# Kernel tuning notes

Measured on AMD Instinct MI355X. Metric: run time of the kernel, lower is better.

The kernel has to match this reference:

```python
import jax, jax.numpy as jnp
import numpy as np

B, S, H, NH = 4, 2048, 1024, 16
HD = H // NH

def setup_inputs() -> dict:
    key = jax.random.key(0)
    ks = jax.random.split(key, 9)
    s = 1.0 / np.sqrt(H)
    return {
        "x": jax.random.normal(ks[0], (B, S, H), dtype=jnp.float32),
        "Wq": jax.random.uniform(ks[1], (H, H), jnp.float32, -s, s),
        "bq": jax.random.uniform(ks[2], (H,), jnp.float32, -s, s),
        "Wk": jax.random.uniform(ks[3], (H, H), jnp.float32, -s, s),
        "bk": jax.random.uniform(ks[4], (H,), jnp.float32, -s, s),
        "Wv": jax.random.uniform(ks[5], (H, H), jnp.float32, -s, s),
        "bv": jax.random.uniform(ks[6], (H,), jnp.float32, -s, s),
        "Wo": jax.random.uniform(ks[7], (H, H), jnp.float32, -s, s),
        "bo": jax.random.uniform(ks[8], (H,), jnp.float32, -s, s),
    }

def reference(x, Wq, bq, Wk, bk, Wv, bv, Wo, bo):
    b, s, h = x.shape
    scale = np.sqrt(HD).astype(np.float32)
    def split_heads(t):  # [b,s,h] -> [b,nh,s,hd]
        return t.reshape(b, s, NH, HD).transpose(0, 2, 1, 3)
    Q = split_heads(x @ Wq.T + bq)
    K = split_heads(x @ Wk.T + bk)
    V = split_heads(x @ Wv.T + bv)
    scores = jnp.einsum('bnqd,bnkd->bnqk', Q, K) / scale
    weights = jax.nn.softmax(scores, axis=-1)
    attn = jnp.einsum('bnqk,bnkd->bnqd', weights, V)
    attn = attn.transpose(0, 2, 1, 3).reshape(b, s, h)
    return attn @ Wo.T + bo
```

## Files before the change

### kernel.cpp

```cpp
#include <hip/hip_runtime.h>
#include <cstdint>

#define BB 4
#define SS 2048
#define HH 1024
#define NHH 16
#define HDD 64

typedef __bf16 bf16x8 __attribute__((ext_vector_type(8)));
typedef float f32x4 __attribute__((ext_vector_type(4)));
typedef unsigned short u16x8 __attribute__((ext_vector_type(8)));

__device__ __forceinline__ unsigned short f2b(float f) {
    unsigned int u = __float_as_uint(f);
    u += 0x7fffu + ((u >> 16) & 1u);
    return (unsigned short)(u >> 16);
}

__device__ __forceinline__ void gload_lds16(const void* g, void* l) {
    __builtin_amdgcn_global_load_lds(
        (const __attribute__((address_space(1))) void*)g,
        (__attribute__((address_space(3))) void*)l, 16, 0, 0);
}

__global__ void cvt_bf16(const float* __restrict__ in,
                         unsigned short* __restrict__ out, long n) {
    long i = ((long)blockIdx.x * blockDim.x + threadIdx.x) * 4;
    long stride = (long)gridDim.x * blockDim.x * 4;
    for (; i < n; i += stride) {
        float4 v = *reinterpret_cast<const float4*>(in + i);
        ushort4 o;
        o.x = f2b(v.x); o.y = f2b(v.y); o.z = f2b(v.z); o.w = f2b(v.w);
        *reinterpret_cast<ushort4*>(out + i) = o;
    }
}

__global__ void cvt_w4(const float* __restrict__ w0, const float* __restrict__ w1,
                       const float* __restrict__ w2, const float* __restrict__ w3,
                       unsigned short* __restrict__ out) {
    const float* s = blockIdx.y == 0 ? w0 : blockIdx.y == 1 ? w1 : blockIdx.y == 2 ? w2 : w3;
    unsigned short* o = out + (size_t)blockIdx.y * ((size_t)HH * HH);
    long n = (long)HH * HH;
    long stride = (long)gridDim.x * blockDim.x * 4;
    for (long i = ((long)blockIdx.x * blockDim.x + threadIdx.x) * 4; i < n; i += stride) {
        float4 v = *reinterpret_cast<const float4*>(s + i);
        ushort4 w;
        w.x = f2b(v.x); w.y = f2b(v.y); w.z = f2b(v.z); w.w = f2b(v.w);
        *reinterpret_cast<ushort4*>(o + i) = w;
    }
}

template<int MODE>
__global__ __launch_bounds__(256) void gemm_bt(
    const unsigned short* __restrict__ A,
    const unsigned short* __restrict__ Bm,
    const float* __restrict__ bias,
    void* __restrict__ Cout,
    int M, int N, int K)
{
    __shared__ alignas(16) unsigned short Al[128][32];
    __shared__ alignas(16) unsigned short Bl[128][32];

    const int tid = threadIdx.x;
    const int lane = tid & 63;
    const int wid  = tid >> 6;
    const int wm = wid >> 1, wn = wid & 1;
    const int l15 = lane & 15, g = lane >> 4;
    const int row0 = blockIdx.y * 128, col0 = blockIdx.x * 128;

    f32x4 acc[4][4];
#pragma unroll
    for (int i = 0; i < 4; i++)
#pragma unroll
        for (int j = 0; j < 4; j++) acc[i][j] = (f32x4)0.0f;

    const int off0 = tid * 16;
    const int r0s = off0 >> 6, cb0 = off0 & 63;
    const int off1 = off0 + 4096;
    const int r1s = off1 >> 6, cb1 = off1 & 63;

    for (int k0 = 0; k0 < K; k0 += 32) {
        const char* gA = (const char*)(A + (size_t)row0 * K + k0);
        const char* gB = (const char*)(Bm + (size_t)col0 * K + k0);
        char* lA = (char*)&Al[0][0] + wid * 1024;
        char* lB = (char*)&Bl[0][0] + wid * 1024;
        gload_lds16(gA + (size_t)r0s * (K * 2) + cb0, lA);
        gload_lds16(gA + (size_t)r1s * (K * 2) + cb1, lA + 4096);
        gload_lds16(gB + (size_t)r0s * (K * 2) + cb0, lB);
        gload_lds16(gB + (size_t)r1s * (K * 2) + cb1, lB + 4096);
        __syncthreads();

        bf16x8 af[4], bf[4];
#pragma unroll
        for (int i = 0; i < 4; i++)
            af[i] = *reinterpret_cast<const bf16x8*>(&Al[wm * 64 + i * 16 + l15][g * 8]);
#pragma unroll
        for (int j = 0; j < 4; j++)
            bf[j] = *reinterpret_cast<const bf16x8*>(&Bl[wn * 64 + j * 16 + l15][g * 8]);
        __builtin_amdgcn_s_setprio(1);
#pragma unroll
        for (int i = 0; i < 4; i++)
#pragma unroll
            for (int j = 0; j < 4; j++)
                acc[i][j] = __builtin_amdgcn_mfma_f32_16x16x32_bf16(af[i], bf[j], acc[i][j], 0, 0, 0);
        __builtin_amdgcn_s_setprio(0);
        __syncthreads();
    }

#pragma unroll
    for (int i = 0; i < 4; i++) {
#pragma unroll
        for (int j = 0; j < 4; j++) {
#pragma unroll
            for (int r = 0; r < 4; r++) {
                int row = row0 + wm * 64 + i * 16 + g * 4 + r;
                int col = col0 + wn * 64 + j * 16 + l15;
                float v = acc[i][j][r] + bias[col];
                if (MODE == 0) {
                    reinterpret_cast<unsigned short*>(Cout)[(size_t)row * N + col] = f2b(v);
                } else if (MODE == 1) {
                    int b = row >> 11;
                    int s = row & (SS - 1);
                    int s6 = s & 63;
                    int sp6 = (s6 & 0x23) | ((s6 & 0x0C) << 1) | ((s6 & 0x10) >> 2);
                    int head = col >> 6;
                    int d = col & (HDD - 1);
                    size_t idx = (((size_t)b * NHH + head) * HDD + d) * SS + (s & ~63) + sp6;
                    reinterpret_cast<unsigned short*>(Cout)[idx] = f2b(v);
                } else {
                    reinterpret_cast<float*>(Cout)[(size_t)row * N + col] = v;
                }
            }
        }
    }
}

__global__ __launch_bounds__(256, 4) void attn_kernel(
    const unsigned short* __restrict__ Q,
    const unsigned short* __restrict__ K,
    const unsigned short* __restrict__ Vt,
    unsigned short* __restrict__ Oa)
{
    __shared__ alignas(16) unsigned short Kl[2][64][72];
    __shared__ alignas(16) unsigned short Vl[2][64][72];

    const int tid = threadIdx.x;
    const int lane = tid & 63;
    const int wid  = tid >> 6;
    const int l15 = lane & 15, g = lane >> 4;

    const int b  = blockIdx.z;
    const int h  = blockIdx.y;
    const int q0 = blockIdx.x * 128;
    const int qA = q0 + wid * 32;

    const float qs = 0.125f * 1.44269504088896f;
    const unsigned short* qpA = Q + (size_t)(b * SS + qA + l15) * HH + h * HDD + g * 8;
    const unsigned short* qpB = qpA + (size_t)16 * HH;
    u16x8 ra0 = *reinterpret_cast<const u16x8*>(qpA);
    u16x8 ra1 = *reinterpret_cast<const u16x8*>(qpA + 32);
    u16x8 rb0 = *reinterpret_cast<const u16x8*>(qpB);
    u16x8 rb1 = *reinterpret_cast<const u16x8*>(qpB + 32);
#pragma unroll
    for (int j = 0; j < 8; j++) {
        ra0[j] = f2b(__uint_as_float((unsigned)ra0[j] << 16) * qs);
        ra1[j] = f2b(__uint_as_float((unsigned)ra1[j] << 16) * qs);
        rb0[j] = f2b(__uint_as_float((unsigned)rb0[j] << 16) * qs);
        rb1[j] = f2b(__uint_as_float((unsigned)rb1[j] << 16) * qs);
    }
    const bf16x8 qa0 = __builtin_bit_cast(bf16x8, ra0);
    const bf16x8 qa1 = __builtin_bit_cast(bf16x8, ra1);
    const bf16x8 qb0 = __builtin_bit_cast(bf16x8, rb0);
    const bf16x8 qb1 = __builtin_bit_cast(bf16x8, rb1);

    u16x8 ou;
#pragma unroll
    for (int j = 0; j < 8; j++) ou[j] = 0x3F80;
    const bf16x8 ones8 = __builtin_bit_cast(bf16x8, ou);
    const f32x4 zero4 = (f32x4)0.0f;

    f32x4 acc_a[4], acc_b[4];
#pragma unroll
    for (int dn = 0; dn < 4; dn++) { acc_a[dn] = zero4; acc_b[dn] = zero4; }
    float m_a = -INFINITY, m_b = -INFINITY, l_a = 0.f, l_b = 0.f;

    const int sr = tid >> 2;
    const int sc = (tid & 3) * 16;

    const unsigned short* gK = K  + (size_t)(b * SS + sr) * HH + h * HDD + sc;
    const unsigned short* gV = Vt + (((size_t)b * NHH + h) * HDD + sr) * SS + sc;

    int4 kr0, kr1, vr0, vr1;

    kr0 = *reinterpret_cast<const int4*>(gK);
    kr1 = *reinterpret_cast<const int4*>(gK + 8);
    vr0 = *reinterpret_cast<const int4*>(gV);
    vr1 = *reinterpret_cast<const int4*>(gV + 8);
    *reinterpret_cast<int4*>(&Kl[0][sr][sc])     = kr0;
    *reinterpret_cast<int4*>(&Kl[0][sr][sc + 8]) = kr1;
    *reinterpret_cast<int4*>(&Vl[0][sr][sc])     = vr0;
    *reinterpret_cast<int4*>(&Vl[0][sr][sc + 8]) = vr1;
    gK += (size_t)64 * HH;
    gV += 64;
    __syncthreads();

    const int NT = SS / 64;
    int cur = 0;

    for (int kt = 0; kt < NT; kt++) {
        if (kt + 1 < NT) {
            kr0 = *reinterpret_cast<const int4*>(gK);
            kr1 = *reinterpret_cast<const int4*>(gK + 8);
            vr0 = *reinterpret_cast<const int4*>(gV);
            vr1 = *reinterpret_cast<const int4*>(gV + 8);
            gK += (size_t)64 * HH;
            gV += 64;
        }

        f32x4 sa[4], sb[4];
        __builtin_amdgcn_s_setprio(1);
#pragma unroll
        for (int n = 0; n < 4; n++) {
            bf16x8 kf0 = *reinterpret_cast<const bf16x8*>(&Kl[cur][n * 16 + l15][g * 8]);
            bf16x8 kf1 = *reinterpret_cast<const bf16x8*>(&Kl[cur][n * 16 + l15][32 + g * 8]);
            sa[n] = __builtin_amdgcn_mfma_f32_16x16x32_bf16(kf0, qa0, zero4, 0, 0, 0);
            sa[n] = __builtin_amdgcn_mfma_f32_16x16x32_bf16(kf1, qa1, sa[n], 0, 0, 0);
            sb[n] = __builtin_amdgcn_mfma_f32_16x16x32_bf16(kf0, qb0, zero4, 0, 0, 0);
            sb[n] = __builtin_amdgcn_mfma_f32_16x16x32_bf16(kf1, qb1, sb[n], 0, 0, 0);
        }
        __builtin_amdgcn_s_setprio(0);

        bf16x8 pa0, pa1, pb0, pb1;
        {
            float u0 = fmaxf(fmaxf(sa[0][0], sa[0][1]), fmaxf(sa[0][2], sa[0][3]));
            float u1 = fmaxf(fmaxf(sa[1][0], sa[1][1]), fmaxf(sa[1][2], sa[1][3]));
            float u2 = fmaxf(fmaxf(sa[2][0], sa[2][1]), fmaxf(sa[2][2], sa[2][3]));
            float u3 = fmaxf(fmaxf(sa[3][0], sa[3][1]), fmaxf(sa[3][2], sa[3][3]));
            float mt = fmaxf(fmaxf(u0, u1), fmaxf(u2, u3));
            mt = fmaxf(mt, __shfl_xor(mt, 16));
            mt = fmaxf(mt, __shfl_xor(mt, 32));
            if (!__all(mt - m_a <= 8.0f)) {
                float mnew = fmaxf(m_a, mt);
                float scl = __builtin_amdgcn_exp2f(m_a - mnew);
                m_a = mnew; l_a *= scl;
#pragma unroll
                for (int dn = 0; dn < 4; dn++)
#pragma unroll
                    for (int r = 0; r < 4; r++) acc_a[dn][r] *= scl;
            }
            float p[4][4];
#pragma unroll
            for (int n = 0; n < 4; n++)
#pragma unroll
                for (int r = 0; r < 4; r++) p[n][r] = __builtin_amdgcn_exp2f(sa[n][r] - m_a);
#pragma unroll
            for (int j = 0; j < 8; j++) {
                pa0[j] = (__bf16)p[j >> 2][j & 3];
                pa1[j] = (__bf16)p[2 + (j >> 2)][j & 3];
            }
        }
        {
            float u0 = fmaxf(fmaxf(sb[0][0], sb[0][1]), fmaxf(sb[0][2], sb[0][3]));
            float u1 = fmaxf(fmaxf(sb[1][0], sb[1][1]), fmaxf(sb[1][2], sb[1][3]));
            float u2 = fmaxf(fmaxf(sb[2][0], sb[2][1]), fmaxf(sb[2][2], sb[2][3]));
            float u3 = fmaxf(fmaxf(sb[3][0], sb[3][1]), fmaxf(sb[3][2], sb[3][3]));
            float mt = fmaxf(fmaxf(u0, u1), fmaxf(u2, u3));
            mt = fmaxf(mt, __shfl_xor(mt, 16));
            mt = fmaxf(mt, __shfl_xor(mt, 32));
            if (!__all(mt - m_b <= 8.0f)) {
                float mnew = fmaxf(m_b, mt);
                float scl = __builtin_amdgcn_exp2f(m_b - mnew);
                m_b = mnew; l_b *= scl;
#pragma unroll
                for (int dn = 0; dn < 4; dn++)
#pragma unroll
                    for (int r = 0; r < 4; r++) acc_b[dn][r] *= scl;
            }
            float p[4][4];
#pragma unroll
            for (int n = 0; n < 4; n++)
#pragma unroll
                for (int r = 0; r < 4; r++) p[n][r] = __builtin_amdgcn_exp2f(sb[n][r] - m_b);
#pragma unroll
            for (int j = 0; j < 8; j++) {
                pb0[j] = (__bf16)p[j >> 2][j & 3];
                pb1[j] = (__bf16)p[2 + (j >> 2)][j & 3];
            }
        }

        f32x4 la = zero4, lb = zero4;
        __builtin_amdgcn_s_setprio(1);
#pragma unroll
        for (int ks = 0; ks < 2; ks++) {
            bf16x8 pA = ks ? pa1 : pa0;
            bf16x8 pB = ks ? pb1 : pb0;
#pragma unroll
            for (int dn = 0; dn < 4; dn++) {
                bf16x8 vf = *reinterpret_cast<const bf16x8*>(&Vl[cur][dn * 16 + l15][ks * 32 + g * 8]);
                acc_a[dn] = __builtin_amdgcn_mfma_f32_16x16x32_bf16(vf, pA, acc_a[dn], 0, 0, 0);
                acc_b[dn] = __builtin_amdgcn_mfma_f32_16x16x32_bf16(vf, pB, acc_b[dn], 0, 0, 0);
            }
        }
        la = __builtin_amdgcn_mfma_f32_16x16x32_bf16(ones8, pa0, la, 0, 0, 0);
        la = __builtin_amdgcn_mfma_f32_16x16x32_bf16(ones8, pa1, la, 0, 0, 0);
        lb = __builtin_amdgcn_mfma_f32_16x16x32_bf16(ones8, pb0, lb, 0, 0, 0);
        lb = __builtin_amdgcn_mfma_f32_16x16x32_bf16(ones8, pb1, lb, 0, 0, 0);
        __builtin_amdgcn_s_setprio(0);
        l_a += la[0];
        l_b += lb[0];

        if (kt + 1 < NT) {
            int nxt = cur ^ 1;
            *reinterpret_cast<int4*>(&Kl[nxt][sr][sc])     = kr0;
            *reinterpret_cast<int4*>(&Kl[nxt][sr][sc + 8]) = kr1;
            *reinterpret_cast<int4*>(&Vl[nxt][sr][sc])     = vr0;
            *reinterpret_cast<int4*>(&Vl[nxt][sr][sc + 8]) = vr1;
        }
        __syncthreads();
        cur ^= 1;
    }

    float inv_a = 1.0f / l_a;
    float inv_b = 1.0f / l_b;
    unsigned short* oA = Oa + (size_t)(b * SS + qA + l15) * HH + h * HDD;
    unsigned short* oB = oA + (size_t)16 * HH;
#pragma unroll
    for (int dn = 0; dn < 4; dn++) {
        ushort4 wa, wb;
        wa.x = f2b(acc_a[dn][0] * inv_a); wa.y = f2b(acc_a[dn][1] * inv_a);
        wa.z = f2b(acc_a[dn][2] * inv_a); wa.w = f2b(acc_a[dn][3] * inv_a);
        wb.x = f2b(acc_b[dn][0] * inv_b); wb.y = f2b(acc_b[dn][1] * inv_b);
        wb.z = f2b(acc_b[dn][2] * inv_b); wb.w = f2b(acc_b[dn][3] * inv_b);
        *reinterpret_cast<ushort4*>(oA + dn * 16 + g * 4) = wa;
        *reinterpret_cast<ushort4*>(oB + dn * 16 + g * 4) = wb;
    }
}

extern "C" void kernel_launch(void* const* d_in, const int* in_sizes, int n_in,
                              void* d_out, int out_size, void* d_ws, size_t ws_size,
                              hipStream_t stream) {
    const float* x  = (const float*)d_in[0];
    const float* Wq = (const float*)d_in[1];
    const float* bq = (const float*)d_in[2];
    const float* Wk = (const float*)d_in[3];
    const float* bk = (const float*)d_in[4];
    const float* Wv = (const float*)d_in[5];
    const float* bv = (const float*)d_in[6];
    const float* Wo = (const float*)d_in[7];
    const float* bo = (const float*)d_in[8];
    float* out = (float*)d_out;

    const int M = BB * SS;
    const long nx = (long)M * HH;

    unsigned char* ws = (unsigned char*)d_ws;
    unsigned short* xb  = (unsigned short*)(ws);
    unsigned short* Wqb = (unsigned short*)(ws + 16777216);
    unsigned short* Wkb = (unsigned short*)(ws + 16777216 + 2097152);
    unsigned short* Wvb = (unsigned short*)(ws + 16777216 + 2 * 2097152);
    unsigned short* Wob = (unsigned short*)(ws + 16777216 + 3 * 2097152);
    unsigned short* Qb  = (unsigned short*)(ws + 16777216 + 4 * 2097152);
    unsigned short* Kb  = (unsigned short*)(ws + 2 * 16777216 + 4 * 2097152);
    unsigned short* Vtb = (unsigned short*)(ws + 3 * 16777216 + 4 * 2097152);
    unsigned short* Ab  = (unsigned short*)(ws + 4 * 16777216 + 4 * 2097152);

    cvt_bf16<<<4096, 256, 0, stream>>>(x, xb, nx);
    cvt_w4<<<dim3(256, 4), 256, 0, stream>>>(Wq, Wk, Wv, Wo, Wqb);

    dim3 ggrid(HH / 128, M / 128);
    gemm_bt<0><<<ggrid, 256, 0, stream>>>(xb, Wqb, bq, Qb, M, HH, HH);
    gemm_bt<0><<<ggrid, 256, 0, stream>>>(xb, Wkb, bk, Kb, M, HH, HH);
    gemm_bt<1><<<ggrid, 256, 0, stream>>>(xb, Wvb, bv, Vtb, M, HH, HH);

    dim3 agrid(SS / 128, NHH, BB);
    attn_kernel<<<agrid, 256, 0, stream>>>(Qb, Kb, Vtb, Ab);

    gemm_bt<2><<<ggrid, 256, 0, stream>>>(Ab, Wob, bo, out, M, HH, HH);
}
```

Before: 222.7 us.

## Fuse QKV projections into one GEMM launch and fragment-order attention LDS tiles

The three separate Q/K/V projection GEMMs become a single launch over a 3x wider N dimension, relying on the contiguous bf16 Wq/Wk/Wv buffers and choosing bias and output layout per column block. This removes two kernel launches and the tail effects of three smaller grids. The attention kernel also stores K and V tiles in LDS in MFMA-fragment order, so each lane reads one contiguous 16-byte slot instead of doing padded row reads. The new LDS write pattern during staging could cause bank conflicts of its own.

```diff
diff --git a/kernel.cpp b/kernel.cpp
--- a/kernel.cpp
+++ b/kernel.cpp
@@ -50,12 +50,101 @@
     }
 }
 
-template<int MODE>
-__global__ __launch_bounds__(256) void gemm_bt(
+__global__ __launch_bounds__(256) void gemm_qkv(
+    const unsigned short* __restrict__ A,
+    const unsigned short* __restrict__ Bqkv,
+    const float* __restrict__ bq, const float* __restrict__ bk,
+    const float* __restrict__ bv,
+    unsigned short* __restrict__ Qo, unsigned short* __restrict__ Ko,
+    unsigned short* __restrict__ Vto)
+{
+    __shared__ alignas(16) unsigned short Al[128][32];
+    __shared__ alignas(16) unsigned short Bl[128][32];
+
+    const int tid = threadIdx.x;
+    const int lane = tid & 63;
+    const int wid  = tid >> 6;
+    const int wm = wid >> 1, wn = wid & 1;
+    const int l15 = lane & 15, g = lane >> 4;
+    const int row0 = blockIdx.y * 128;
+    const int col0 = blockIdx.x * 128;
+    const int nb = col0 >> 10;
+    const int cbase = col0 & 1023;
+    const float* bias = nb == 0 ? bq : nb == 1 ? bk : bv;
+    const int K = HH;
+
+    f32x4 acc[4][4];
+#pragma unroll
+    for (int i = 0; i < 4; i++)
+#pragma unroll
+        for (int j = 0; j < 4; j++) acc[i][j] = (f32x4)0.0f;
+
+    const int off0 = tid * 16;
+    const int r0s = off0 >> 6, cb0 = off0 & 63;
+    const int off1 = off0 + 4096;
+    const int r1s = off1 >> 6, cb1 = off1 & 63;
+
+    for (int k0 = 0; k0 < K; k0 += 32) {
+        const char* gA = (const char*)(A + (size_t)row0 * K + k0);
+        const char* gB = (const char*)(Bqkv + (size_t)col0 * K + k0);
+        char* lA = (char*)&Al[0][0] + wid * 1024;
+        char* lB = (char*)&Bl[0][0] + wid * 1024;
+        gload_lds16(gA + (size_t)r0s * (K * 2) + cb0, lA);
+        gload_lds16(gA + (size_t)r1s * (K * 2) + cb1, lA + 4096);
+        gload_lds16(gB + (size_t)r0s * (K * 2) + cb0, lB);
+        gload_lds16(gB + (size_t)r1s * (K * 2) + cb1, lB + 4096);
+        __syncthreads();
+
+        bf16x8 af[4], bf[4];
+#pragma unroll
+        for (int i = 0; i < 4; i++)
+            af[i] = *reinterpret_cast<const bf16x8*>(&Al[wm * 64 + i * 16 + l15][g * 8]);
+#pragma unroll
+        for (int j = 0; j < 4; j++)
+            bf[j] = *reinterpret_cast<const bf16x8*>(&Bl[wn * 64 + j * 16 + l15][g * 8]);
+        __builtin_amdgcn_s_setprio(1);
+#pragma unroll
+        for (int i = 0; i < 4; i++)
+#pragma unroll
+            for (int j = 0; j < 4; j++)
+                acc[i][j] = __builtin_amdgcn_mfma_f32_16x16x32_bf16(af[i], bf[j], acc[i][j], 0, 0, 0);
+        __builtin_amdgcn_s_setprio(0);
+        __syncthreads();
+    }
+
+#pragma unroll
+    for (int i = 0; i < 4; i++) {
+#pragma unroll
+        for (int j = 0; j < 4; j++) {
+#pragma unroll
+            for (int r = 0; r < 4; r++) {
+                int row = row0 + wm * 64 + i * 16 + g * 4 + r;
+                int col = cbase + wn * 64 + j * 16 + l15;
+                float v = acc[i][j][r] + bias[col];
+                if (nb == 0) {
+                    Qo[(size_t)row * HH + col] = f2b(v);
+                } else if (nb == 1) {
+                    Ko[(size_t)row * HH + col] = f2b(v);
+                } else {
+                    int b = row >> 11;
+                    int s = row & (SS - 1);
+                    int s6 = s & 63;
+                    int sp6 = (s6 & 0x23) | ((s6 & 0x0C) << 1) | ((s6 & 0x10) >> 2);
+                    int head = col >> 6;
+                    int d = col & (HDD - 1);
+                    size_t idx = (((size_t)b * NHH + head) * HDD + d) * SS + (s & ~63) + sp6;
+                    Vto[idx] = f2b(v);
+                }
+            }
+        }
+    }
+}
+
+__global__ __launch_bounds__(256) void gemm_out(
     const unsigned short* __restrict__ A,
     const unsigned short* __restrict__ Bm,
     const float* __restrict__ bias,
-    void* __restrict__ Cout,
+    float* __restrict__ Cout,
     int M, int N, int K)
 {
     __shared__ alignas(16) unsigned short Al[128][32];
@@ -115,21 +204,7 @@
             for (int r = 0; r < 4; r++) {
                 int row = row0 + wm * 64 + i * 16 + g * 4 + r;
                 int col = col0 + wn * 64 + j * 16 + l15;
-                float v = acc[i][j][r] + bias[col];
-                if (MODE == 0) {
-                    reinterpret_cast<unsigned short*>(Cout)[(size_t)row * N + col] = f2b(v);
-                } else if (MODE == 1) {
-                    int b = row >> 11;
-                    int s = row & (SS - 1);
-                    int s6 = s & 63;
-                    int sp6 = (s6 & 0x23) | ((s6 & 0x0C) << 1) | ((s6 & 0x10) >> 2);
-                    int head = col >> 6;
-                    int d = col & (HDD - 1);
-                    size_t idx = (((size_t)b * NHH + head) * HDD + d) * SS + (s & ~63) + sp6;
-                    reinterpret_cast<unsigned short*>(Cout)[idx] = f2b(v);
-                } else {
-                    reinterpret_cast<float*>(Cout)[(size_t)row * N + col] = v;
-                }
+                Cout[(size_t)row * N + col] = acc[i][j][r] + bias[col];
             }
         }
     }
@@ -141,8 +216,8 @@
     const unsigned short* __restrict__ Vt,
     unsigned short* __restrict__ Oa)
 {
-    __shared__ alignas(16) unsigned short Kl[2][64][72];
-    __shared__ alignas(16) unsigned short Vl[2][64][72];
+    __shared__ alignas(16) unsigned short Kf[2][8][64][8];
+    __shared__ alignas(16) unsigned short Vf[2][8][64][8];
 
     const int tid = threadIdx.x;
     const int lane = tid & 63;
@@ -184,22 +259,30 @@
     for (int dn = 0; dn < 4; dn++) { acc_a[dn] = zero4; acc_b[dn] = zero4; }
     float m_a = -INFINITY, m_b = -INFINITY, l_a = 0.f, l_b = 0.f;
 
-    const int sr = tid >> 2;
-    const int sc = (tid & 3) * 16;
-
-    const unsigned short* gK = K  + (size_t)(b * SS + sr) * HH + h * HDD + sc;
-    const unsigned short* gV = Vt + (((size_t)b * NHH + h) * HDD + sr) * SS + sc;
+    const int srow = tid >> 2;
+    const int d0a  = (tid & 3) * 2;
+    const int sfrag = ((srow >> 4) << 1) + (d0a >> 2);
+    const int sslot = (srow & 15) | ((d0a & 3) << 4);
+
+    const unsigned short* gK = K  + (size_t)(b * SS + srow) * HH + h * HDD + d0a * 8;
+    const unsigned short* gV = Vt + (((size_t)b * NHH + h) * HDD + srow) * SS + d0a * 8;
 
     int4 kr0, kr1, vr0, vr1;
+
+    auto stage_write = [&](int buf) {
+        unsigned short* pk = &Kf[buf][sfrag][0][0] + sslot * 8;
+        unsigned short* pv = &Vf[buf][sfrag][0][0] + sslot * 8;
+        *reinterpret_cast<int4*>(pk)       = kr0;
+        *reinterpret_cast<int4*>(pk + 128) = kr1;
+        *reinterpret_cast<int4*>(pv)       = vr0;
+        *reinterpret_cast<int4*>(pv + 128) = vr1;
+    };
 
     kr0 = *reinterpret_cast<const int4*>(gK);
     kr1 = *reinterpret_cast<const int4*>(gK + 8);
     vr0 = *reinterpret_cast<const int4*>(gV);
     vr1 = *reinterpret_cast<const int4*>(gV + 8);
-    *reinterpret_cast<int4*>(&Kl[0][sr][sc])     = kr0;
-    *reinterpret_cast<int4*>(&Kl[0][sr][sc + 8]) = kr1;
-    *reinterpret_cast<int4*>(&Vl[0][sr][sc])     = vr0;
-    *reinterpret_cast<int4*>(&Vl[0][sr][sc + 8]) = vr1;
+    stage_write(0);
     gK += (size_t)64 * HH;
     gV += 64;
     __syncthreads();
@@ -221,8 +304,8 @@
         __builtin_amdgcn_s_setprio(1);
 #pragma unroll
         for (int n = 0; n < 4; n++) {
-            bf16x8 kf0 = *reinterpret_cast<const bf16x8*>(&Kl[cur][n * 16 + l15][g * 8]);
-            bf16x8 kf1 = *reinterpret_cast<const bf16x8*>(&Kl[cur][n * 16 + l15][32 + g * 8]);
+            bf16x8 kf0 = *reinterpret_cast<const bf16x8*>(&Kf[cur][n * 2 + 0][lane][0]);
+            bf16x8 kf1 = *reinterpret_cast<const bf16x8*>(&Kf[cur][n * 2 + 1][lane][0]);
             sa[n] = __builtin_amdgcn_mfma_f32_16x16x32_bf16(kf0, qa0, zero4, 0, 0, 0);
             sa[n] = __builtin_amdgcn_mfma_f32_16x16x32_bf16(kf1, qa1, sa[n], 0, 0, 0);
             sb[n] = __builtin_amdgcn_mfma_f32_16x16x32_bf16(kf0, qb0, zero4, 0, 0, 0);
@@ -296,7 +379,7 @@
             bf16x8 pB = ks ? pb1 : pb0;
 #pragma unroll
             for (int dn = 0; dn < 4; dn++) {
-                bf16x8 vf = *reinterpret_cast<const bf16x8*>(&Vl[cur][dn * 16 + l15][ks * 32 + g * 8]);
+                bf16x8 vf = *reinterpret_cast<const bf16x8*>(&Vf[cur][dn * 2 + ks][lane][0]);
                 acc_a[dn] = __builtin_amdgcn_mfma_f32_16x16x32_bf16(vf, pA, acc_a[dn], 0, 0, 0);
                 acc_b[dn] = __builtin_amdgcn_mfma_f32_16x16x32_bf16(vf, pB, acc_b[dn], 0, 0, 0);
             }
@@ -309,13 +392,7 @@
         l_a += la[0];
         l_b += lb[0];
 
-        if (kt + 1 < NT) {
-            int nxt = cur ^ 1;
-            *reinterpret_cast<int4*>(&Kl[nxt][sr][sc])     = kr0;
-            *reinterpret_cast<int4*>(&Kl[nxt][sr][sc + 8]) = kr1;
-            *reinterpret_cast<int4*>(&Vl[nxt][sr][sc])     = vr0;
-            *reinterpret_cast<int4*>(&Vl[nxt][sr][sc + 8]) = vr1;
-        }
+        if (kt + 1 < NT) stage_write(cur ^ 1);
         __syncthreads();
         cur ^= 1;
     }
@@ -356,8 +433,6 @@
     unsigned char* ws = (unsigned char*)d_ws;
     unsigned short* xb  = (unsigned short*)(ws);
     unsigned short* Wqb = (unsigned short*)(ws + 16777216);
-    unsigned short* Wkb = (unsigned short*)(ws + 16777216 + 2097152);
-    unsigned short* Wvb = (unsigned short*)(ws + 16777216 + 2 * 2097152);
     unsigned short* Wob = (unsigned short*)(ws + 16777216 + 3 * 2097152);
     unsigned short* Qb  = (unsigned short*)(ws + 16777216 + 4 * 2097152);
     unsigned short* Kb  = (unsigned short*)(ws + 2 * 16777216 + 4 * 2097152);
@@ -367,13 +442,12 @@
     cvt_bf16<<<4096, 256, 0, stream>>>(x, xb, nx);
     cvt_w4<<<dim3(256, 4), 256, 0, stream>>>(Wq, Wk, Wv, Wo, Wqb);
 
-    dim3 ggrid(HH / 128, M / 128);
-    gemm_bt<0><<<ggrid, 256, 0, stream>>>(xb, Wqb, bq, Qb, M, HH, HH);
-    gemm_bt<0><<<ggrid, 256, 0, stream>>>(xb, Wkb, bk, Kb, M, HH, HH);
-    gemm_bt<1><<<ggrid, 256, 0, stream>>>(xb, Wvb, bv, Vtb, M, HH, HH);
+    dim3 qgrid(3 * HH / 128, M / 128);
+    gemm_qkv<<<qgrid, 256, 0, stream>>>(xb, Wqb, bq, bk, bv, Qb, Kb, Vtb);
 
     dim3 agrid(SS / 128, NHH, BB);
     attn_kernel<<<agrid, 256, 0, stream>>>(Qb, Kb, Vtb, Ab);
 
-    gemm_bt<2><<<ggrid, 256, 0, stream>>>(Ab, Wob, bo, out, M, HH, HH);
-}
+    dim3 ogrid(HH / 128, M / 128);
+    gemm_out<<<ogrid, 256, 0, stream>>>(Ab, Wob, bo, out, M, HH, HH);
+}
```

Result: no change. 223.5 us (+0.3%).

## Triple-buffer GEMM loads with fragment-ordered LDS, and fragment-layout attention tiles

Applied to the files above, without the earlier changes.

The projection GEMM now uses a three-stage LDS ring with async global-to-LDS loads issued two tiles ahead and manual vmcnt waits in place of full syncthreads. LDS tiles are stored in MFMA fragment order so each lane reads one contiguous 16-byte chunk. The attention kernel stores K and V in the same fragment-ordered layout to avoid padded rows and bank conflicts. It also remaps a flat 1D grid so each group of consecutive blocks cycles over heads, aimed at better cache or XCD locality. The risks are more LDS per block, which may lower occupancy, and fragile hand-counted waitcnt values.

```diff
diff --git a/kernel.cpp b/kernel.cpp
--- a/kernel.cpp
+++ b/kernel.cpp
@@ -51,22 +51,25 @@
 }
 
 template<int MODE>
-__global__ __launch_bounds__(256) void gemm_bt(
+__global__ __launch_bounds__(256) void gemm_proj(
     const unsigned short* __restrict__ A,
     const unsigned short* __restrict__ Bm,
     const float* __restrict__ bias,
-    void* __restrict__ Cout,
-    int M, int N, int K)
+    void* __restrict__ Cout)
 {
-    __shared__ alignas(16) unsigned short Al[128][32];
-    __shared__ alignas(16) unsigned short Bl[128][32];
+    __shared__ alignas(16) unsigned short Al[3][4096];
+    __shared__ alignas(16) unsigned short Bl[3][4096];
 
     const int tid = threadIdx.x;
     const int lane = tid & 63;
     const int wid  = tid >> 6;
     const int wm = wid >> 1, wn = wid & 1;
     const int l15 = lane & 15, g = lane >> 4;
-    const int row0 = blockIdx.y * 128, col0 = blockIdx.x * 128;
+
+    const int col0 = blockIdx.x * 128;
+    const int row0 = blockIdx.y * 128;
+    const int K = HH;
+    const int K2 = K * 2;
 
     f32x4 acc[4][4];
 #pragma unroll
@@ -74,37 +77,57 @@
 #pragma unroll
         for (int j = 0; j < 4; j++) acc[i][j] = (f32x4)0.0f;
 
-    const int off0 = tid * 16;
-    const int r0s = off0 >> 6, cb0 = off0 & 63;
-    const int off1 = off0 + 4096;
-    const int r1s = off1 >> 6, cb1 = off1 & 63;
-
-    for (int k0 = 0; k0 < K; k0 += 32) {
-        const char* gA = (const char*)(A + (size_t)row0 * K + k0);
-        const char* gB = (const char*)(Bm + (size_t)col0 * K + k0);
-        char* lA = (char*)&Al[0][0] + wid * 1024;
-        char* lB = (char*)&Bl[0][0] + wid * 1024;
-        gload_lds16(gA + (size_t)r0s * (K * 2) + cb0, lA);
-        gload_lds16(gA + (size_t)r1s * (K * 2) + cb1, lA + 4096);
-        gload_lds16(gB + (size_t)r0s * (K * 2) + cb0, lB);
-        gload_lds16(gB + (size_t)r1s * (K * 2) + cb1, lB + 4096);
-        __syncthreads();
-
+    const int goff0 = (wid * 16 + l15) * K2 + g * 16;
+    const int goff1 = ((4 + wid) * 16 + l15) * K2 + g * 16;
+
+    const char* gAb = (const char*)(A + (size_t)row0 * K);
+    const char* gBb = (const char*)(Bm + (size_t)col0 * K);
+
+    char* Abase = (char*)&Al[0][0];
+    char* Bbase = (char*)&Bl[0][0];
+
+    auto STAGE = [&](int off, int t) {
+        const char* a = gAb + t * 64;
+        const char* bsrc = gBb + t * 64;
+        gload_lds16(a + goff0, Abase + off + wid * 1024);
+        gload_lds16(a + goff1, Abase + off + 4096 + wid * 1024);
+        gload_lds16(bsrc + goff0, Bbase + off + wid * 1024);
+        gload_lds16(bsrc + goff1, Bbase + off + 4096 + wid * 1024);
+    };
+
+    int o0 = 0, o1 = 8192, o2 = 16384;
+    STAGE(o0, 0);
+    STAGE(o1, 1);
+
+    for (int k = 0; k < 32; k++) {
+        if (k < 30) {
+            STAGE(o2, k + 2);
+            asm volatile("s_waitcnt vmcnt(8)" ::: "memory");
+        } else if (k == 30) {
+            asm volatile("s_waitcnt vmcnt(4)" ::: "memory");
+        } else {
+            asm volatile("s_waitcnt vmcnt(0)" ::: "memory");
+        }
+        __builtin_amdgcn_s_barrier();
+
+        const char* Ac = Abase + o0;
+        const char* Bc = Bbase + o0;
         bf16x8 af[4], bf[4];
 #pragma unroll
         for (int i = 0; i < 4; i++)
-            af[i] = *reinterpret_cast<const bf16x8*>(&Al[wm * 64 + i * 16 + l15][g * 8]);
+            af[i] = *reinterpret_cast<const bf16x8*>(Ac + (wm * 4 + i) * 1024 + lane * 16);
 #pragma unroll
         for (int j = 0; j < 4; j++)
-            bf[j] = *reinterpret_cast<const bf16x8*>(&Bl[wn * 64 + j * 16 + l15][g * 8]);
-        __builtin_amdgcn_s_setprio(1);
+            bf[j] = *reinterpret_cast<const bf16x8*>(Bc + (wn * 4 + j) * 1024 + lane * 16);
 #pragma unroll
         for (int i = 0; i < 4; i++)
 #pragma unroll
             for (int j = 0; j < 4; j++)
                 acc[i][j] = __builtin_amdgcn_mfma_f32_16x16x32_bf16(af[i], bf[j], acc[i][j], 0, 0, 0);
-        __builtin_amdgcn_s_setprio(0);
-        __syncthreads();
+
+        __builtin_amdgcn_s_barrier();
+
+        int t = o0; o0 = o1; o1 = o2; o2 = t;
     }
 
 #pragma unroll
@@ -117,7 +140,7 @@
                 int col = col0 + wn * 64 + j * 16 + l15;
                 float v = acc[i][j][r] + bias[col];
                 if (MODE == 0) {
-                    reinterpret_cast<unsigned short*>(Cout)[(size_t)row * N + col] = f2b(v);
+                    reinterpret_cast<unsigned short*>(Cout)[(size_t)row * HH + col] = f2b(v);
                 } else if (MODE == 1) {
                     int b = row >> 11;
                     int s = row & (SS - 1);
@@ -128,7 +151,7 @@
                     size_t idx = (((size_t)b * NHH + head) * HDD + d) * SS + (s & ~63) + sp6;
                     reinterpret_cast<unsigned short*>(Cout)[idx] = f2b(v);
                 } else {
-                    reinterpret_cast<float*>(Cout)[(size_t)row * N + col] = v;
+                    reinterpret_cast<float*>(Cout)[(size_t)row * HH + col] = v;
                 }
             }
         }
@@ -141,17 +164,21 @@
     const unsigned short* __restrict__ Vt,
     unsigned short* __restrict__ Oa)
 {
-    __shared__ alignas(16) unsigned short Kl[2][64][72];
-    __shared__ alignas(16) unsigned short Vl[2][64][72];
+    __shared__ alignas(16) unsigned short Kf[2][8][64][8];
+    __shared__ alignas(16) unsigned short Vf[2][8][64][8];
 
     const int tid = threadIdx.x;
     const int lane = tid & 63;
     const int wid  = tid >> 6;
     const int l15 = lane & 15, g = lane >> 4;
 
-    const int b  = blockIdx.z;
-    const int h  = blockIdx.y;
-    const int q0 = blockIdx.x * 128;
+    const int wg = blockIdx.x;
+    const int L = (wg & 7) * 128 + (wg >> 3);
+    const int qt = L & 15;
+    const int bh = L >> 4;
+    const int b  = bh >> 4;
+    const int h  = bh & 15;
+    const int q0 = qt * 128;
     const int qA = q0 + wid * 32;
 
     const float qs = 0.125f * 1.44269504088896f;
@@ -184,22 +211,30 @@
     for (int dn = 0; dn < 4; dn++) { acc_a[dn] = zero4; acc_b[dn] = zero4; }
     float m_a = -INFINITY, m_b = -INFINITY, l_a = 0.f, l_b = 0.f;
 
-    const int sr = tid >> 2;
-    const int sc = (tid & 3) * 16;
-
-    const unsigned short* gK = K  + (size_t)(b * SS + sr) * HH + h * HDD + sc;
-    const unsigned short* gV = Vt + (((size_t)b * NHH + h) * HDD + sr) * SS + sc;
+    const int srow = tid >> 2;
+    const int d0a  = (tid & 3) * 2;
+    const int sfrag = ((srow >> 4) << 1) + (d0a >> 2);
+    const int sslot = (srow & 15) | ((d0a & 3) << 4);
+
+    const unsigned short* gK = K  + (size_t)(b * SS + srow) * HH + h * HDD + d0a * 8;
+    const unsigned short* gV = Vt + (((size_t)b * NHH + h) * HDD + srow) * SS + d0a * 8;
 
     int4 kr0, kr1, vr0, vr1;
+
+    auto stage_write = [&](int buf) {
+        unsigned short* pk = &Kf[buf][sfrag][0][0] + sslot * 8;
+        unsigned short* pv = &Vf[buf][sfrag][0][0] + sslot * 8;
+        *reinterpret_cast<int4*>(pk)       = kr0;
+        *reinterpret_cast<int4*>(pk + 128) = kr1;
+        *reinterpret_cast<int4*>(pv)       = vr0;
+        *reinterpret_cast<int4*>(pv + 128) = vr1;
+    };
 
     kr0 = *reinterpret_cast<const int4*>(gK);
     kr1 = *reinterpret_cast<const int4*>(gK + 8);
     vr0 = *reinterpret_cast<const int4*>(gV);
     vr1 = *reinterpret_cast<const int4*>(gV + 8);
-    *reinterpret_cast<int4*>(&Kl[0][sr][sc])     = kr0;
-    *reinterpret_cast<int4*>(&Kl[0][sr][sc + 8]) = kr1;
-    *reinterpret_cast<int4*>(&Vl[0][sr][sc])     = vr0;
-    *reinterpret_cast<int4*>(&Vl[0][sr][sc + 8]) = vr1;
+    stage_write(0);
     gK += (size_t)64 * HH;
     gV += 64;
     __syncthreads();
@@ -221,8 +256,8 @@
         __builtin_amdgcn_s_setprio(1);
 #pragma unroll
         for (int n = 0; n < 4; n++) {
-            bf16x8 kf0 = *reinterpret_cast<const bf16x8*>(&Kl[cur][n * 16 + l15][g * 8]);
-            bf16x8 kf1 = *reinterpret_cast<const bf16x8*>(&Kl[cur][n * 16 + l15][32 + g * 8]);
+            bf16x8 kf0 = *reinterpret_cast<const bf16x8*>(&Kf[cur][n * 2 + 0][lane][0]);
+            bf16x8 kf1 = *reinterpret_cast<const bf16x8*>(&Kf[cur][n * 2 + 1][lane][0]);
             sa[n] = __builtin_amdgcn_mfma_f32_16x16x32_bf16(kf0, qa0, zero4, 0, 0, 0);
             sa[n] = __builtin_amdgcn_mfma_f32_16x16x32_bf16(kf1, qa1, sa[n], 0, 0, 0);
             sb[n] = __builtin_amdgcn_mfma_f32_16x16x32_bf16(kf0, qb0, zero4, 0, 0, 0);
@@ -296,7 +331,7 @@
             bf16x8 pB = ks ? pb1 : pb0;
 #pragma unroll
             for (int dn = 0; dn < 4; dn++) {
-                bf16x8 vf = *reinterpret_cast<const bf16x8*>(&Vl[cur][dn * 16 + l15][ks * 32 + g * 8]);
+                bf16x8 vf = *reinterpret_cast<const bf16x8*>(&Vf[cur][dn * 2 + ks][lane][0]);
                 acc_a[dn] = __builtin_amdgcn_mfma_f32_16x16x32_bf16(vf, pA, acc_a[dn], 0, 0, 0);
                 acc_b[dn] = __builtin_amdgcn_mfma_f32_16x16x32_bf16(vf, pB, acc_b[dn], 0, 0, 0);
             }
@@ -309,13 +344,7 @@
         l_a += la[0];
         l_b += lb[0];
 
-        if (kt + 1 < NT) {
-            int nxt = cur ^ 1;
-            *reinterpret_cast<int4*>(&Kl[nxt][sr][sc])     = kr0;
-            *reinterpret_cast<int4*>(&Kl[nxt][sr][sc + 8]) = kr1;
-            *reinterpret_cast<int4*>(&Vl[nxt][sr][sc])     = vr0;
-            *reinterpret_cast<int4*>(&Vl[nxt][sr][sc + 8]) = vr1;
-        }
+        if (kt + 1 < NT) stage_write(cur ^ 1);
         __syncthreads();
         cur ^= 1;
     }
@@ -368,12 +397,11 @@
     cvt_w4<<<dim3(256, 4), 256, 0, stream>>>(Wq, Wk, Wv, Wo, Wqb);
 
     dim3 ggrid(HH / 128, M / 128);
-    gemm_bt<0><<<ggrid, 256, 0, stream>>>(xb, Wqb, bq, Qb, M, HH, HH);
-    gemm_bt<0><<<ggrid, 256, 0, stream>>>(xb, Wkb, bk, Kb, M, HH, HH);
-    gemm_bt<1><<<ggrid, 256, 0, stream>>>(xb, Wvb, bv, Vtb, M, HH, HH);
-
-    dim3 agrid(SS / 128, NHH, BB);
-    attn_kernel<<<agrid, 256, 0, stream>>>(Qb, Kb, Vtb, Ab);
-
-    gemm_bt<2><<<ggrid, 256, 0, stream>>>(Ab, Wob, bo, out, M, HH, HH);
-}
+    gemm_proj<0><<<ggrid, 256, 0, stream>>>(xb, Wqb, bq, Qb);
+    gemm_proj<0><<<ggrid, 256, 0, stream>>>(xb, Wkb, bk, Kb);
+    gemm_proj<1><<<ggrid, 256, 0, stream>>>(xb, Wvb, bv, Vtb);
+
+    attn_kernel<<<1024, 256, 0, stream>>>(Qb, Kb, Vtb, Ab);
+
+    gemm_proj<2><<<ggrid, 256, 0, stream>>>(Ab, Wob, bo, out);
+}
```

New measurement: 255.4 us. 1.15x slower.

## Stage attention K/V tiles via direct global-to-LDS loads with fragment layout

Applied to the files above, without the earlier changes.

The attention kernel now loads K and V tiles straight into LDS with global_load_lds, using a fragment-major layout so each lane reads its MFMA operand contiguously. Explicit vmcnt waits and raw barriers replace the register round-trip and __syncthreads. The grid is flattened to 1D with a remap that spreads consecutive workgroups across batch and head, likely to improve cache and XCD locality. The GEMM is specialised with compile-time K and N. Risks include LDS bank conflicts in the new layout and a fragile waitcnt count.

```diff
diff --git a/kernel.cpp b/kernel.cpp
--- a/kernel.cpp
+++ b/kernel.cpp
@@ -51,12 +51,11 @@
 }
 
 template<int MODE>
-__global__ __launch_bounds__(256) void gemm_bt(
+__global__ __launch_bounds__(256) void gemm_proj(
     const unsigned short* __restrict__ A,
     const unsigned short* __restrict__ Bm,
     const float* __restrict__ bias,
-    void* __restrict__ Cout,
-    int M, int N, int K)
+    void* __restrict__ Cout)
 {
     __shared__ alignas(16) unsigned short Al[128][32];
     __shared__ alignas(16) unsigned short Bl[128][32];
@@ -67,6 +66,7 @@
     const int wm = wid >> 1, wn = wid & 1;
     const int l15 = lane & 15, g = lane >> 4;
     const int row0 = blockIdx.y * 128, col0 = blockIdx.x * 128;
+    const int K = HH;
 
     f32x4 acc[4][4];
 #pragma unroll
@@ -117,7 +117,7 @@
                 int col = col0 + wn * 64 + j * 16 + l15;
                 float v = acc[i][j][r] + bias[col];
                 if (MODE == 0) {
-                    reinterpret_cast<unsigned short*>(Cout)[(size_t)row * N + col] = f2b(v);
+                    reinterpret_cast<unsigned short*>(Cout)[(size_t)row * HH + col] = f2b(v);
                 } else if (MODE == 1) {
                     int b = row >> 11;
                     int s = row & (SS - 1);
@@ -128,7 +128,7 @@
                     size_t idx = (((size_t)b * NHH + head) * HDD + d) * SS + (s & ~63) + sp6;
                     reinterpret_cast<unsigned short*>(Cout)[idx] = f2b(v);
                 } else {
-                    reinterpret_cast<float*>(Cout)[(size_t)row * N + col] = v;
+                    reinterpret_cast<float*>(Cout)[(size_t)row * HH + col] = v;
                 }
             }
         }
@@ -141,17 +141,21 @@
     const unsigned short* __restrict__ Vt,
     unsigned short* __restrict__ Oa)
 {
-    __shared__ alignas(16) unsigned short Kl[2][64][72];
-    __shared__ alignas(16) unsigned short Vl[2][64][72];
+    __shared__ alignas(16) unsigned short Kf[2][8][64][8];
+    __shared__ alignas(16) unsigned short Vf[2][8][64][8];
 
     const int tid = threadIdx.x;
     const int lane = tid & 63;
     const int wid  = tid >> 6;
     const int l15 = lane & 15, g = lane >> 4;
 
-    const int b  = blockIdx.z;
-    const int h  = blockIdx.y;
-    const int q0 = blockIdx.x * 128;
+    const int wg = blockIdx.x;
+    const int L = (wg & 7) * 128 + (wg >> 3);
+    const int qt = L & 15;
+    const int bh = L >> 4;
+    const int b  = bh >> 4;
+    const int h  = bh & 15;
+    const int q0 = qt * 128;
     const int qA = q0 + wid * 32;
 
     const float qs = 0.125f * 1.44269504088896f;
@@ -184,45 +188,40 @@
     for (int dn = 0; dn < 4; dn++) { acc_a[dn] = zero4; acc_b[dn] = zero4; }
     float m_a = -INFINITY, m_b = -INFINITY, l_a = 0.f, l_b = 0.f;
 
-    const int sr = tid >> 2;
-    const int sc = (tid & 3) * 16;
-
-    const unsigned short* gK = K  + (size_t)(b * SS + sr) * HH + h * HDD + sc;
-    const unsigned short* gV = Vt + (((size_t)b * NHH + h) * HDD + sr) * SS + sc;
-
-    int4 kr0, kr1, vr0, vr1;
-
-    kr0 = *reinterpret_cast<const int4*>(gK);
-    kr1 = *reinterpret_cast<const int4*>(gK + 8);
-    vr0 = *reinterpret_cast<const int4*>(gV);
-    vr1 = *reinterpret_cast<const int4*>(gV + 8);
-    *reinterpret_cast<int4*>(&Kl[0][sr][sc])     = kr0;
-    *reinterpret_cast<int4*>(&Kl[0][sr][sc + 8]) = kr1;
-    *reinterpret_cast<int4*>(&Vl[0][sr][sc])     = vr0;
-    *reinterpret_cast<int4*>(&Vl[0][sr][sc + 8]) = vr1;
-    gK += (size_t)64 * HH;
-    gV += 64;
-    __syncthreads();
+    const int krow = wid * 16 + l15;
+    const unsigned short* gKs = K  + (size_t)(b * SS + krow) * HH + h * HDD + (lane >> 4) * 8;
+    const unsigned short* gVs = Vt + (((size_t)b * NHH + h) * HDD + krow) * SS + (lane >> 4) * 8;
+    char* kdst = (char*)&Kf[0][2 * wid][0][0];
+    char* vdst = (char*)&Vf[0][2 * wid][0][0];
+
+    auto STAGE = [&](int buf, int kt) {
+        const unsigned short* pk = gKs + (size_t)(kt * 64) * HH;
+        const unsigned short* pv = gVs + kt * 64;
+        gload_lds16(pk,      kdst + buf * 8192);
+        gload_lds16(pk + 32, kdst + buf * 8192 + 1024);
+        gload_lds16(pv,      vdst + buf * 8192);
+        gload_lds16(pv + 32, vdst + buf * 8192 + 1024);
+    };
 
     const int NT = SS / 64;
+    STAGE(0, 0);
     int cur = 0;
 
     for (int kt = 0; kt < NT; kt++) {
         if (kt + 1 < NT) {
-            kr0 = *reinterpret_cast<const int4*>(gK);
-            kr1 = *reinterpret_cast<const int4*>(gK + 8);
-            vr0 = *reinterpret_cast<const int4*>(gV);
-            vr1 = *reinterpret_cast<const int4*>(gV + 8);
-            gK += (size_t)64 * HH;
-            gV += 64;
-        }
+            STAGE(cur ^ 1, kt + 1);
+            asm volatile("s_waitcnt vmcnt(4)" ::: "memory");
+        } else {
+            asm volatile("s_waitcnt vmcnt(0)" ::: "memory");
+        }
+        __builtin_amdgcn_s_barrier();
 
         f32x4 sa[4], sb[4];
         __builtin_amdgcn_s_setprio(1);
 #pragma unroll
         for (int n = 0; n < 4; n++) {
-            bf16x8 kf0 = *reinterpret_cast<const bf16x8*>(&Kl[cur][n * 16 + l15][g * 8]);
-            bf16x8 kf1 = *reinterpret_cast<const bf16x8*>(&Kl[cur][n * 16 + l15][32 + g * 8]);
+            bf16x8 kf0 = *reinterpret_cast<const bf16x8*>(&Kf[cur][n * 2 + 0][lane][0]);
+            bf16x8 kf1 = *reinterpret_cast<const bf16x8*>(&Kf[cur][n * 2 + 1][lane][0]);
             sa[n] = __builtin_amdgcn_mfma_f32_16x16x32_bf16(kf0, qa0, zero4, 0, 0, 0);
             sa[n] = __builtin_amdgcn_mfma_f32_16x16x32_bf16(kf1, qa1, sa[n], 0, 0, 0);
             sb[n] = __builtin_amdgcn_mfma_f32_16x16x32_bf16(kf0, qb0, zero4, 0, 0, 0);
@@ -296,7 +295,7 @@
             bf16x8 pB = ks ? pb1 : pb0;
 #pragma unroll
             for (int dn = 0; dn < 4; dn++) {
-                bf16x8 vf = *reinterpret_cast<const bf16x8*>(&Vl[cur][dn * 16 + l15][ks * 32 + g * 8]);
+                bf16x8 vf = *reinterpret_cast<const bf16x8*>(&Vf[cur][dn * 2 + ks][lane][0]);
                 acc_a[dn] = __builtin_amdgcn_mfma_f32_16x16x32_bf16(vf, pA, acc_a[dn], 0, 0, 0);
                 acc_b[dn] = __builtin_amdgcn_mfma_f32_16x16x32_bf16(vf, pB, acc_b[dn], 0, 0, 0);
             }
@@ -309,14 +308,7 @@
         l_a += la[0];
         l_b += lb[0];
 
-        if (kt + 1 < NT) {
-            int nxt = cur ^ 1;
-            *reinterpret_cast<int4*>(&Kl[nxt][sr][sc])     = kr0;
-            *reinterpret_cast<int4*>(&Kl[nxt][sr][sc + 8]) = kr1;
-            *reinterpret_cast<int4*>(&Vl[nxt][sr][sc])     = vr0;
-            *reinterpret_cast<int4*>(&Vl[nxt][sr][sc + 8]) = vr1;
-        }
-        __syncthreads();
+        __builtin_amdgcn_s_barrier();
         cur ^= 1;
     }
 
@@ -368,12 +360,11 @@
     cvt_w4<<<dim3(256, 4), 256, 0, stream>>>(Wq, Wk, Wv, Wo, Wqb);
 
     dim3 ggrid(HH / 128, M / 128);
-    gemm_bt<0><<<ggrid, 256, 0, stream>>>(xb, Wqb, bq, Qb, M, HH, HH);
-    gemm_bt<0><<<ggrid, 256, 0, stream>>>(xb, Wkb, bk, Kb, M, HH, HH);
-    gemm_bt<1><<<ggrid, 256, 0, stream>>>(xb, Wvb, bv, Vtb, M, HH, HH);
-
-    dim3 agrid(SS / 128, NHH, BB);
-    attn_kernel<<<agrid, 256, 0, stream>>>(Qb, Kb, Vtb, Ab);
-
-    gemm_bt<2><<<ggrid, 256, 0, stream>>>(Ab, Wob, bo, out, M, HH, HH);
-}
+    gemm_proj<0><<<ggrid, 256, 0, stream>>>(xb, Wqb, bq, Qb);
+    gemm_proj<0><<<ggrid, 256, 0, stream>>>(xb, Wkb, bk, Kb);
+    gemm_proj<1><<<ggrid, 256, 0, stream>>>(xb, Wvb, bv, Vtb);
+
+    attn_kernel<<<1024, 256, 0, stream>>>(Qb, Kb, Vtb, Ab);
+
+    gemm_proj<2><<<ggrid, 256, 0, stream>>>(Ab, Wob, bo, out);
+}
```

New measurement: 227.7 us. 1.02x slower.
